# Kernel optimization log

Measured on AMD Instinct MI355X. Metric: run time of the kernel, lower is better.

## Reference

```python
import jax, jax.numpy as jnp
from jax import lax
import numpy as np

S, B, T, N, FJ, H, MF, M = 8, 64, 64, 16, 32, 128, 16, 8
NN = S + M  # total machine-graph nodes
EPS = 1e-5
SLOPE = 0.2


def layernorm(x, g, b):
    mu = x.mean(-1, keepdims=True)
    var = ((x - mu) ** 2).mean(-1, keepdims=True)
    return (x - mu) / jnp.sqrt(var + EPS) * g + b


def gat(adj, x, W, a):
    # dense GAT layer: x [..., N, Fin], adj [..., N, N]
    h = x @ W  # [..., N, O]
    O = W.shape[1]
    f1 = h @ a[:O]  # [..., N]
    f2 = h @ a[O:]
    e = jax.nn.leaky_relu(f1[..., :, None] + f2[..., None, :], SLOPE)
    e = jnp.where(adj > 0, e, jnp.float32(-1e9))
    return jax.nn.softmax(e, axis=-1) @ h


def job_enc(adj, x, Ws, As):
    t = jnp.tanh(gat(adj, x, Ws[0], As[0]))
    t = jnp.tanh(gat(adj, t, Ws[1], As[1]) + t)
    t = jnp.tanh(gat(adj, t, Ws[2], As[2]) + t)
    t = jnp.tanh(t + gat(adj, t, Ws[3], As[3]))
    return t.mean(-2)  # mean over ops dim


def lstm_last(x, Wih, Whh, b):
    # x: [Bx, T, H]; returns final hidden state [Bx, H]
    xs = jnp.einsum('bti,gi->tbg', x, Wih) + b  # [T, Bx, 4H]
    h0 = jnp.zeros((x.shape[0], Whh.shape[1]), x.dtype)

    def step(carry, xt):
        h, c = carry
        g = xt + h @ Whh.T
        i, f, gg, o = jnp.split(g, 4, axis=-1)
        c = jax.nn.sigmoid(f) * c + jax.nn.sigmoid(i) * jnp.tanh(gg)
        h = jax.nn.sigmoid(o) * jnp.tanh(c)
        return (h, c), None

    (h, _), _ = lax.scan(step, (h0, h0), xs)
    return h


def setup_inputs() -> dict:
    key = jax.random.key(0)
    ks = jax.random.split(key, 32)

    def adj(k, shape):
        a = jax.random.bernoulli(k, 0.4, shape).astype(jnp.int32)
        return jnp.maximum(a, jnp.eye(shape[-1], dtype=jnp.int32))

    mfeat = jax.random.normal(ks[4], (B, NN, MF), jnp.float32)
    # stage nodes (first S) have feature[...,0] > 0; machine nodes < 0
    mfeat = mfeat.at[:, :S, 0].set(jnp.abs(mfeat[:, :S, 0]) + 0.1)
    mfeat = mfeat.at[:, S:, 0].set(-jnp.abs(mfeat[:, S:, 0]) - 0.1)

    sc = 0.08
    inp = {
        'j_stages_f': jax.random.normal(ks[0], (S, B, T, N, FJ), jnp.float32),
        'j_stages_a': adj(ks[1], (S, B, T, N, N)),
        'j_machine_f': jax.random.normal(ks[2], (B, M, N, FJ), jnp.float32),
        'j_machine_a': adj(ks[3], (B, M, N, N)),
        'machine_f': mfeat,
        'machine_a': adj(ks[5], (B, NN, NN)),
        'jg1_W': jax.random.normal(ks[6], (FJ, H), jnp.float32) * sc,
        'jgW': jax.random.normal(ks[7], (3, H, H), jnp.float32) * sc,
        'jga': jax.random.normal(ks[8], (4, 2 * H), jnp.float32) * sc,
        'lstm_Wih': jax.random.normal(ks[9], (4 * H, H), jnp.float32) * sc,
        'lstm_Whh': jax.random.normal(ks[10], (4 * H, H), jnp.float32) * sc,
        'lstm_b': jnp.zeros((4 * H,), jnp.float32),
        'mfe_W': jax.random.normal(ks[11], (MF, H), jnp.float32) * sc,
        'mfe_b': jnp.zeros((H,), jnp.float32),
        'n2_g': jnp.ones((H,), jnp.float32),
        'n2_b': jnp.zeros((H,), jnp.float32),
        'me_W': jax.random.normal(ks[12], (2 * H, H), jnp.float32) * sc,
        'me_b': jnp.zeros((H,), jnp.float32),
        'n3_g': jnp.ones((H,), jnp.float32),
        'n3_b': jnp.zeros((H,), jnp.float32),
        'mgW': jax.random.normal(ks[13], (4, H, H), jnp.float32) * sc,
        'mga': jax.random.normal(ks[14], (4, 2 * H), jnp.float32) * sc,
        'mng': jnp.ones((4, H), jnp.float32),
        'mnb': jnp.zeros((4, H), jnp.float32),
    }
    return inp


def reference(j_stages_f, j_stages_a, j_machine_f, j_machine_a, machine_f,
              machine_a, jg1_W, jgW, jga, lstm_Wih, lstm_Whh, lstm_b,
              mfe_W, mfe_b, n2_g, n2_b, me_W, me_b, n3_g, n3_b,
              mgW, mga, mng, mnb):
    Ws = [jg1_W, jgW[0], jgW[1], jgW[2]]
    As = [jga[0], jga[1], jga[2], jga[3]]

    # per-stage job encoding + LSTM over job sequence
    stage_emb = jax.vmap(lambda a, f: job_enc(a, f, Ws, As))(j_stages_a, j_stages_f)  # [S,B,T,H]
    hlast = lstm_last(stage_emb.reshape(S * B, T, H), lstm_Wih, lstm_Whh, lstm_b)
    j_encoded = hlast.reshape(S, B, H).transpose(1, 0, 2)  # [B,S,H]

    # machine-side job graph encoding (shared encoder)
    jm = job_enc(j_machine_a, j_machine_f, Ws, As)  # [B,M,H]

    # machine node embedding
    mfh = jnp.tanh(layernorm(machine_f @ mfe_W + mfe_b, n2_g, n2_b))  # [B,NN,H]

    # static routing: first S nodes -> stage contexts, rest -> machine contexts
    ctx = jnp.concatenate([j_encoded, jm], axis=1)  # [B,NN,H]
    nodes = jnp.concatenate([mfh, ctx], axis=-1)  # [B,NN,2H]
    nodes = jnp.tanh(layernorm(nodes @ me_W + me_b, n3_g, n3_b))

    h = nodes
    prev = None
    for k in range(4):
        h2 = layernorm(gat(machine_a, h, mgW[k], mga[k]), mng[k], mnb[k])
        if k != 0:
            h2 = h2 + prev
        h = jnp.tanh(h2)
        prev = h
    return h.mean(axis=1)  # [B, H]
```

## Files before the change

kernel.cpp:

```cpp
#include <hip/hip_runtime.h>
#include <hip/hip_bf16.h>
#include <math.h>

#define S_ 8
#define B_ 64
#define T_ 64
#define N_ 16
#define FJ_ 32
#define H_ 128
#define MF_ 16
#define M_ 8
#define SB_ 512
#define G1_ 32768
#define G2_ 512

#define CPAD 132
#define PPAD 17

typedef short bf16x8 __attribute__((ext_vector_type(8)));
typedef short bf16x4 __attribute__((ext_vector_type(4)));
typedef float f32x4 __attribute__((ext_vector_type(4)));
typedef unsigned short u16;

__device__ __forceinline__ u16 f2bf(float f) {
  union { float f; unsigned u; } v; v.f = f;
  unsigned r = v.u + 0x7FFFu + ((v.u >> 16) & 1u);
  return (u16)(r >> 16);
}
__device__ __forceinline__ unsigned pk2(float lo, float hi) {
  __hip_bfloat162 h2 = __float22bfloat162_rn(make_float2(lo, hi));
  union { __hip_bfloat162 h; unsigned u; } x; x.h = h2; return x.u;
}
__device__ __forceinline__ bf16x4 mkfrag(unsigned a, unsigned b) {
  union { bf16x4 v; unsigned u[2]; } x; x.u[0] = a; x.u[1] = b; return x.v;
}
__device__ __forceinline__ f32x4 mfma16(bf16x4 a, bf16x4 b, f32x4 c) {
#if __has_builtin(__builtin_amdgcn_mfma_f32_16x16x16bf16_1k)
  return __builtin_amdgcn_mfma_f32_16x16x16bf16_1k(a, b, c, 0, 0, 0);
#else
  asm("v_mfma_f32_16x16x16_bf16 %0, %1, %2, %0" : "+v"(c) : "v"(a), "v"(b));
  return c;
#endif
}
__device__ __forceinline__ float frcp(float x) {
#if __has_builtin(__builtin_amdgcn_rcpf)
  return __builtin_amdgcn_rcpf(x);
#else
  return 1.f / x;
#endif
}
__device__ __forceinline__ float frsq(float x) {
#if __has_builtin(__builtin_amdgcn_rsqf)
  return __builtin_amdgcn_rsqf(x);
#else
  return rsqrtf(x);
#endif
}
__device__ __forceinline__ float ftanh(float x) {
  float e = __expf(2.f * x);
  return fmaf(-2.f, frcp(e + 1.f), 1.f);
}
__device__ __forceinline__ float sigmoidf_(float x) {
  return frcp(1.f + __expf(-x));
}

__device__ __forceinline__ void fma8(float (&acc)[8], float xv, float4 wa, float4 wb) {
  acc[0] = fmaf(xv, wa.x, acc[0]); acc[1] = fmaf(xv, wa.y, acc[1]);
  acc[2] = fmaf(xv, wa.z, acc[2]); acc[3] = fmaf(xv, wa.w, acc[3]);
  acc[4] = fmaf(xv, wb.x, acc[4]); acc[5] = fmaf(xv, wb.y, acc[5]);
  acc[6] = fmaf(xv, wb.z, acc[6]); acc[7] = fmaf(xv, wb.w, acc[7]);
}
__device__ __forceinline__ float grp16_sum(float v) {
#pragma unroll
  for (int m = 1; m < 16; m <<= 1) v += __shfl_xor(v, m);
  return v;
}
__device__ __forceinline__ float grp16_max(float v) {
#pragma unroll
  for (int m = 1; m < 16; m <<= 1) v = fmaxf(v, __shfl_xor(v, m));
  return v;
}
__device__ __forceinline__ void ln_row(float (&v)[8], const float* gw, const float* bw, int j0) {
  float s1 = 0.f, s2 = 0.f;
#pragma unroll
  for (int c = 0; c < 8; ++c) { s1 += v[c]; s2 += v[c] * v[c]; }
  s1 = grp16_sum(s1); s2 = grp16_sum(s2);
  float mu = s1 * (1.f / 128.f);
  float var = s2 * (1.f / 128.f) - mu * mu;
  float rstd = frsq(var + 1e-5f);
#pragma unroll
  for (int c = 0; c < 8; ++c) v[c] = (v[c] - mu) * rstd * gw[j0 + c] + bw[j0 + c];
}

__global__ __launch_bounds__(256) void pack_w_kernel(
    const float* __restrict__ W0, const float* __restrict__ W123,
    const float* __restrict__ jga,
    const float* __restrict__ Wih, const float* __restrict__ Whh,
    u16* __restrict__ wpk0, u16* __restrict__ wpkL,
    u16* __restrict__ wpkIH, u16* __restrict__ wpkHH)
{
  int idx = blockIdx.x * 256 + threadIdx.x;
  if (idx < 4608) {
    int e = idx & 3, l = (idx >> 2) & 63, t = idx >> 8;
    int n = t >> 1, kk = t & 1;
    int q = l >> 4, cc = l & 15;
    int k = 16 * kk + 4 * q + e;
    float v = 0.f;
    if (n < 8) v = W0[k * 128 + 16 * n + cc];
    else if (cc < 2) {
      const float* a = jga + cc * 128;
      float s = 0.f;
      for (int j = 0; j < 128; ++j) s += W0[k * 128 + j] * a[j];
      v = s;
    }
    wpk0[idx] = f2bf(v);
  } else if (idx < 59904) {
    int id = idx - 4608;
    int e = id & 3, l = (id >> 2) & 63;
    int t2 = id >> 8;
    int t = t2 % 72, layer = t2 / 72;
    int n = t >> 3, kk = t & 7;
    int q = l >> 4, cc = l & 15;
    int k = 16 * kk + 4 * q + e;
    const float* W = W123 + (size_t)layer * 16384;
    float v = 0.f;
    if (n < 8) v = W[k * 128 + 16 * n + cc];
    else if (cc < 2) {
      const float* a = jga + (layer + 1) * 256 + cc * 128;
      float s = 0.f;
      for (int j = 0; j < 128; ++j) s += W[k * 128 + j] * a[j];
      v = s;
    }
    wpkL[id] = f2bf(v);
  } else if (idx < 125440) {
    int id = idx - 59904;
    int e = id & 7, l = (id >> 3) & 63, kk = (id >> 9) & 3, n = id >> 11;
    int gate = 16 * n + (l & 15), k = 32 * kk + 8 * (l >> 4) + e;
    wpkIH[id] = f2bf(Wih[gate * 128 + k]);
  } else if (idx < 190976) {
    int id = idx - 125440;
    int e = id & 7, l = (id >> 3) & 63, kk = (id >> 9) & 3, n = id >> 11;
    int gate = 16 * n + (l & 15), k = 32 * kk + 8 * (l >> 4) + e;
    wpkHH[id] = f2bf(Whh[gate * 128 + k]);
  }
}

__global__ __launch_bounds__(512) __attribute__((amdgpu_waves_per_eu(2, 4)))
void gat_mfma_kernel(
    const float* __restrict__ xinA,
    const int* __restrict__ adjA,
    float* __restrict__ outmA, u16* __restrict__ outbfA,
    const float* __restrict__ xinB,
    const int* __restrict__ adjB,
    float* __restrict__ outmB, u16* __restrict__ outbfB,
    const u16* __restrict__ wpk0, const u16* __restrict__ wpkL)
{
  __shared__ __align__(16) u16 wbuf[18432];
  __shared__ __align__(16) float fbuf[8][32];

  const int wv = threadIdx.x >> 6;
  const int l = threadIdx.x & 63;
  const int c = l & 15, q = l >> 4;
  float* fb = fbuf[wv];

  const float* xin; const int* adjin; float* outm; u16* outbf; int g;
  if (blockIdx.x < G1_ / 8) {
    xin = xinA; adjin = adjA; outm = outmA; outbf = outbfA;
    g = blockIdx.x * 8 + wv;
  } else {
    xin = xinB; adjin = adjB; outm = outmB; outbf = outbfB;
    g = (blockIdx.x - G1_ / 8) * 8 + wv;
  }

  auto stage = [&](const u16* src, int nbytes) {
    const float4* s4 = (const float4*)src;
    float4* d4 = (float4*)wbuf;
    int n16 = nbytes >> 4;
    for (int i = threadIdx.x; i < n16; i += 512) d4[i] = s4[i];
  };

  int4 A1 = *(const int4*)(adjin + (size_t)g * 256 + c * 16 + 4 * q);

  f32x4 res[8];
  bf16x4 hfrag[8];

  auto softmax_pv = [&](f32x4 Cf, bool resid) {
    if (c < 2) *(f32x4*)(fb + c * 16 + 4 * q) = Cf;
    float f1v = fb[c];
    float4 f2v = *(const float4*)(fb + 16 + 4 * q);
    float ev[4] = {f1v + f2v.x, f1v + f2v.y, f1v + f2v.z, f1v + f2v.w};
#pragma unroll
    for (int e = 0; e < 4; ++e) ev[e] = (ev[e] >= 0.f) ? ev[e] : 0.2f * ev[e];
    ev[0] = (A1.x > 0) ? ev[0] : -1e9f;
    ev[1] = (A1.y > 0) ? ev[1] : -1e9f;
    ev[2] = (A1.z > 0) ? ev[2] : -1e9f;
    ev[3] = (A1.w > 0) ? ev[3] : -1e9f;
    float mx = fmaxf(fmaxf(ev[0], ev[1]), fmaxf(ev[2], ev[3]));
    mx = fmaxf(mx, __shfl_xor(mx, 16));
    mx = fmaxf(mx, __shfl_xor(mx, 32));
    float sm = 0.f;
#pragma unroll
    for (int e = 0; e < 4; ++e) { ev[e] = __expf(ev[e] - mx); sm += ev[e]; }
    sm += __shfl_xor(sm, 16);
    sm += __shfl_xor(sm, 32);
    float zinv = frcp(sm);
    bf16x4 pfrag = mkfrag(pk2(ev[0] * zinv, ev[1] * zinv), pk2(ev[2] * zinv, ev[3] * zinv));
#pragma unroll
    for (int m = 0; m < 8; ++m) {
      f32x4 o = resid ? res[m] : (f32x4){0.f, 0.f, 0.f, 0.f};
      o = mfma16(hfrag[m], pfrag, o);
      f32x4 t;
      t[0] = ftanh(o[0]); t[1] = ftanh(o[1]); t[2] = ftanh(o[2]); t[3] = ftanh(o[3]);
      res[m] = t;
    }
  };

  stage(wpk0, 9216);
  __syncthreads();
  {
    bf16x4 xf[2];
    const float* xg = xin + (size_t)g * 512 + c * 32 + 4 * q;
    float4 x1 = *(const float4*)xg;
    float4 x2 = *(const float4*)(xg + 16);
    xf[0] = mkfrag(pk2(x1.x, x1.y), pk2(x1.z, x1.w));
    xf[1] = mkfrag(pk2(x2.x, x2.y), pk2(x2.z, x2.w));
#pragma unroll
    for (int n = 0; n < 8; ++n) {
      f32x4 Ch = (f32x4){0.f, 0.f, 0.f, 0.f};
#pragma unroll
      for (int kk = 0; kk < 2; ++kk) {
        bf16x4 wf = *(const bf16x4*)(wbuf + ((n * 2 + kk) * 64 + l) * 4);
        Ch = mfma16(xf[kk], wf, Ch);
      }
      hfrag[n] = mkfrag(pk2(Ch[0], Ch[1]), pk2(Ch[2], Ch[3]));
    }
    f32x4 Cf = (f32x4){0.f, 0.f, 0.f, 0.f};
#pragma unroll
    for (int kk = 0; kk < 2; ++kk) {
      bf16x4 wf = *(const bf16x4*)(wbuf + ((16 + kk) * 64 + l) * 4);
      Cf = mfma16(xf[kk], wf, Cf);
    }
    softmax_pv(Cf, false);
  }
  __syncthreads();

#pragma unroll 1
  for (int layer = 1; layer < 4; ++layer) {
    stage(wpkL + (size_t)(layer - 1) * 18432, 36864);
    __syncthreads();
    bf16x4 xf[8];
#pragma unroll
    for (int kk = 0; kk < 8; ++kk)
      xf[kk] = mkfrag(pk2(res[kk][0], res[kk][1]), pk2(res[kk][2], res[kk][3]));
#pragma unroll
    for (int n = 0; n < 8; ++n) {
      f32x4 Ch = (f32x4){0.f, 0.f, 0.f, 0.f};
#pragma unroll
      for (int kk = 0; kk < 8; ++kk) {
        bf16x4 wf = *(const bf16x4*)(wbuf + ((n * 8 + kk) * 64 + l) * 4);
        Ch = mfma16(xf[kk], wf, Ch);
      }
      hfrag[n] = mkfrag(pk2(Ch[0], Ch[1]), pk2(Ch[2], Ch[3]));
    }
    f32x4 Cf = (f32x4){0.f, 0.f, 0.f, 0.f};
#pragma unroll
    for (int kk = 0; kk < 8; ++kk) {
      bf16x4 wf = *(const bf16x4*)(wbuf + ((64 + kk) * 64 + l) * 4);
      Cf = mfma16(xf[kk], wf, Cf);
    }
    softmax_pv(Cf, true);
    __syncthreads();
  }

  u16* tb = wbuf + wv * 2176;
#pragma unroll
  for (int m = 0; m < 8; ++m) {
    uint2 u;
    u.x = pk2(res[m][0], res[m][1]);
    u.y = pk2(res[m][2], res[m][3]);
    *(uint2*)(tb + c * 136 + 16 * m + 4 * q) = u;
  }
  {
    float s0 = 0.f, s1 = 0.f;
#pragma unroll
    for (int node = 0; node < 16; ++node) {
      unsigned u = *(const unsigned*)(tb + node * 136 + 2 * l);
      union { unsigned u; float f; } lo, hi;
      lo.u = u << 16; hi.u = u & 0xffff0000u;
      s0 += lo.f; s1 += hi.f;
    }
    s0 *= 0.0625f; s1 *= 0.0625f;
    *(float2*)(outm + (size_t)g * 128 + 2 * l) = make_float2(s0, s1);
    *(unsigned*)(outbf + (size_t)g * 128 + 2 * l) = pk2(s0, s1);
  }
}

__global__ __launch_bounds__(512) __attribute__((amdgpu_waves_per_eu(1, 2)))
void lstm_fused_kernel(
    const u16* __restrict__ emb_bf,
    const u16* __restrict__ wpkIH, const u16* __restrict__ wpkHH,
    const float* __restrict__ bvec,
    float* __restrict__ hlast)
{
  __shared__ unsigned hbuf[2][1024];
  const int tid = threadIdx.x;
  const int w = tid >> 6, l = tid & 63;
  const int c = l & 15, q = l >> 4;
  const int seq0 = blockIdx.x * 16;
  const int swz = (c & 7) << 2;

  bf16x8 aih[4][4], ahh[4][4];
#pragma unroll
  for (int m = 0; m < 4; ++m)
#pragma unroll
    for (int kk = 0; kk < 4; ++kk) {
      int n = 8 * m + w;
      aih[m][kk] = *(const bf16x8*)(wpkIH + ((size_t)((n * 4 + kk) * 64 + l)) * 8);
      ahh[m][kk] = *(const bf16x8*)(wpkHH + ((size_t)((n * 4 + kk) * 64 + l)) * 8);
    }
  float bias[4][4];
#pragma unroll
  for (int m = 0; m < 4; ++m)
#pragma unroll
    for (int r = 0; r < 4; ++r) bias[m][r] = bvec[128 * m + 16 * w + 4 * q + r];

  hbuf[0][tid] = 0u;
  hbuf[0][512 + tid] = 0u;
  __syncthreads();

  const u16* xbase = emb_bf + ((size_t)(seq0 + c)) * 64 * 128 + q * 8;

  f32x4 accih[4];
  {
    bf16x8 xf[4];
#pragma unroll
    for (int kk = 0; kk < 4; ++kk) xf[kk] = *(const bf16x8*)(xbase + kk * 32);
#pragma unroll
    for (int m = 0; m < 4; ++m) {
      f32x4 a = (f32x4){0.f, 0.f, 0.f, 0.f};
#pragma unroll
      for (int kk = 0; kk < 4; ++kk)
        a = __builtin_amdgcn_mfma_f32_16x16x32_bf16(aih[m][kk], xf[kk], a, 0, 0, 0);
      accih[m] = a;
    }
  }

  float cst[4] = {0.f, 0.f, 0.f, 0.f};
  float hv[4] = {0.f, 0.f, 0.f, 0.f};
  int pb = 0;
#pragma unroll 1
  for (int t = 0; t < T_; ++t) {
    bf16x8 hf[4];
#pragma unroll
    for (int kk = 0; kk < 4; ++kk) {
      int j0 = (16 * kk + 4 * q) ^ swz;
      hf[kk] = *(const bf16x8*)&hbuf[pb][c * 64 + j0];
    }
    f32x4 acc[4];
#pragma unroll
    for (int m = 0; m < 4; ++m) {
      f32x4 a = accih[m];
#pragma unroll
      for (int kk = 0; kk < 4; ++kk)
        a = __builtin_amdgcn_mfma_f32_16x16x32_bf16(ahh[m][kk], hf[kk], a, 0, 0, 0);
      acc[m] = a;
    }
#pragma unroll
    for (int r = 0; r < 4; ++r) {
      float ig = acc[0][r] + bias[0][r];
      float fg = acc[1][r] + bias[1][r];
      float gg = acc[2][r] + bias[2][r];
      float og = acc[3][r] + bias[3][r];
      cst[r] = sigmoidf_(fg) * cst[r] + sigmoidf_(ig) * ftanh(gg);
      hv[r] = sigmoidf_(og) * ftanh(cst[r]);
    }
    {
      int j0 = (8 * w + 2 * q) ^ swz;
      uint2 u2; u2.x = pk2(hv[0], hv[1]); u2.y = pk2(hv[2], hv[3]);
      *(uint2*)&hbuf[pb ^ 1][c * 64 + j0] = u2;
    }
    __syncthreads();
    pb ^= 1;
    if (t < T_ - 1) {
      bf16x8 xf[4];
      const u16* xr = xbase + (t + 1) * 128;
#pragma unroll
      for (int kk = 0; kk < 4; ++kk) xf[kk] = *(const bf16x8*)(xr + kk * 32);
#pragma unroll
      for (int m = 0; m < 4; ++m) {
        f32x4 a = (f32x4){0.f, 0.f, 0.f, 0.f};
#pragma unroll
        for (int kk = 0; kk < 4; ++kk)
          a = __builtin_amdgcn_mfma_f32_16x16x32_bf16(aih[m][kk], xf[kk], a, 0, 0, 0);
        accih[m] = a;
      }
    }
  }
#pragma unroll
  for (int r = 0; r < 4; ++r)
    hlast[((size_t)(seq0 + c)) * 128 + 16 * w + 4 * q + r] = hv[r];
}

__global__ __launch_bounds__(256) __attribute__((amdgpu_waves_per_eu(2, 4)))
void machine_kernel(
    const float* __restrict__ machine_f, const int* __restrict__ machine_a,
    const float* __restrict__ hlast, const float* __restrict__ jm,
    const float* __restrict__ mfe_W, const float* __restrict__ mfe_b,
    const float* __restrict__ n2_g, const float* __restrict__ n2_b,
    const float* __restrict__ me_W, const float* __restrict__ me_b,
    const float* __restrict__ n3_g, const float* __restrict__ n3_b,
    const float* __restrict__ mgW, const float* __restrict__ mga,
    const float* __restrict__ mng, const float* __restrict__ mnb,
    float* __restrict__ outp)
{
  __shared__ float mf[256];
  __shared__ int adjs[256];
  __shared__ __align__(16) float ctx[16 * CPAD];
  __shared__ __align__(16) float mfh[16 * CPAD];
  __shared__ __align__(16) float cur[16 * CPAD];
  __shared__ __align__(16) float tmp[16 * CPAD];
  __shared__ __align__(16) float prevb[16 * CPAD];
  __shared__ float pm[16 * PPAD];
  __shared__ float f1s[16], f2s[16];

  const int b = blockIdx.x;
  const int tid = threadIdx.x;
  const int i = tid >> 4;
  const int jb = tid & 15;
  const int j0 = jb << 3;

  mf[tid] = machine_f[(size_t)b * 256 + tid];
  adjs[tid] = machine_a[(size_t)b * 256 + tid];
  {
    const float* src = (i < 8) ? (hlast + ((size_t)i * B_ + b) * H_)
                               : (jm + ((size_t)b * M_ + (i - 8)) * H_);
    *(float4*)(ctx + i * CPAD + j0) = ((const float4*)src)[jb * 2];
    *(float4*)(ctx + i * CPAD + j0 + 4) = ((const float4*)src)[jb * 2 + 1];
  }
  __syncthreads();

  {
    float acc[8];
#pragma unroll
    for (int c = 0; c < 8; ++c) acc[c] = 0.f;
#pragma unroll
    for (int k = 0; k < MF_; ++k) {
      float xv = mf[i * 16 + k];
      float4 wa = *(const float4*)(mfe_W + (size_t)k * H_ + j0);
      float4 wb = *(const float4*)(mfe_W + (size_t)k * H_ + j0 + 4);
      fma8(acc, xv, wa, wb);
    }
#pragma unroll
    for (int c = 0; c < 8; ++c) acc[c] += mfe_b[j0 + c];
    ln_row(acc, n2_g, n2_b, j0);
#pragma unroll
    for (int c = 0; c < 8; ++c) mfh[i * CPAD + j0 + c] = ftanh(acc[c]);
  }
  __syncthreads();

  {
    float acc[8];
#pragma unroll
    for (int c = 0; c < 8; ++c) acc[c] = 0.f;
#pragma unroll 4
    for (int k = 0; k < H_; ++k) {
      float xv = mfh[i * CPAD + k];
      float4 wa = *(const float4*)(me_W + (size_t)k * H_ + j0);
      float4 wb = *(const float4*)(me_W + (size_t)k * H_ + j0 + 4);
      fma8(acc, xv, wa, wb);
    }
#pragma unroll 4
    for (int k = 0; k < H_; ++k) {
      float xv = ctx[i * CPAD + k];
      float4 wa = *(const float4*)(me_W + (size_t)(128 + k) * H_ + j0);
      float4 wb = *(const float4*)(me_W + (size_t)(128 + k) * H_ + j0 + 4);
      fma8(acc, xv, wa, wb);
    }
#pragma unroll
    for (int c = 0; c < 8; ++c) acc[c] += me_b[j0 + c];
    ln_row(acc, n3_g, n3_b, j0);
#pragma unroll
    for (int c = 0; c < 8; ++c) cur[i * CPAD + j0 + c] = ftanh(acc[c]);
  }
  __syncthreads();

  for (int l = 0; l < 4; ++l) {
    const float* W = mgW + (size_t)l * H_ * H_;
    const float* a0 = mga + l * 256;
    const float* a1 = a0 + 128;

    float acc[8];
#pragma unroll
    for (int c = 0; c < 8; ++c) acc[c] = 0.f;
#pragma unroll 4
    for (int k = 0; k < H_; ++k) {
      float xv = cur[i * CPAD + k];
      float4 wa = *(const float4*)(W + (size_t)k * H_ + j0);
      float4 wb = *(const float4*)(W + (size_t)k * H_ + j0 + 4);
      fma8(acc, xv, wa, wb);
    }
    *(float4*)(tmp + i * CPAD + j0) = make_float4(acc[0], acc[1], acc[2], acc[3]);
    *(float4*)(tmp + i * CPAD + j0 + 4) = make_float4(acc[4], acc[5], acc[6], acc[7]);

    float p1 = 0.f, p2 = 0.f;
#pragma unroll
    for (int c = 0; c < 8; ++c) {
      p1 = fmaf(acc[c], a0[j0 + c], p1);
      p2 = fmaf(acc[c], a1[j0 + c], p2);
    }
    p1 = grp16_sum(p1); p2 = grp16_sum(p2);
    if (jb == 0) { f1s[i] = p1; f2s[i] = p2; }
    __syncthreads();

    {
      int jc = jb;
      float e = f1s[i] + f2s[jc];
      e = (e >= 0.f) ? e : 0.2f * e;
      if (adjs[i * 16 + jc] <= 0) e = -1e9f;
      float mxv = grp16_max(e);
      float ex = __expf(e - mxv);
      float smv = grp16_sum(ex);
      pm[i * PPAD + jc] = ex * frcp(smv);
    }
    __syncthreads();

    float o[8];
#pragma unroll
    for (int c = 0; c < 8; ++c) o[c] = 0.f;
#pragma unroll
    for (int k = 0; k < 16; ++k) {
      float pv = pm[i * PPAD + k];
      float4 ha = *(const float4*)(tmp + k * CPAD + j0);
      float4 hb = *(const float4*)(tmp + k * CPAD + j0 + 4);
      fma8(o, pv, ha, hb);
    }
    ln_row(o, mng + l * H_, mnb + l * H_, j0);
#pragma unroll
    for (int c = 0; c < 8; ++c) {
      float v = o[c] + ((l > 0) ? prevb[i * CPAD + j0 + c] : 0.f);
      v = ftanh(v);
      cur[i * CPAD + j0 + c] = v;
      prevb[i * CPAD + j0 + c] = v;
    }
    __syncthreads();
  }

  if (tid < 128) {
    float s = 0.f;
#pragma unroll
    for (int r = 0; r < 16; ++r) s += cur[r * CPAD + tid];
    outp[(size_t)b * H_ + tid] = s * (1.f / 16.f);
  }
}

extern "C" void kernel_launch(void* const* d_in, const int* in_sizes, int n_in,
                              void* d_out, int out_size, void* d_ws, size_t ws_size,
                              hipStream_t stream) {
  const float* j_stages_f  = (const float*)d_in[0];
  const int*   j_stages_a  = (const int*)d_in[1];
  const float* j_machine_f = (const float*)d_in[2];
  const int*   j_machine_a = (const int*)d_in[3];
  const float* machine_f   = (const float*)d_in[4];
  const int*   machine_a   = (const int*)d_in[5];
  const float* jg1_W       = (const float*)d_in[6];
  const float* jgW         = (const float*)d_in[7];
  const float* jga         = (const float*)d_in[8];
  const float* lstm_Wih    = (const float*)d_in[9];
  const float* lstm_Whh    = (const float*)d_in[10];
  const float* lstm_b      = (const float*)d_in[11];
  const float* mfe_W       = (const float*)d_in[12];
  const float* mfe_b       = (const float*)d_in[13];
  const float* n2_g        = (const float*)d_in[14];
  const float* n2_b        = (const float*)d_in[15];
  const float* me_W        = (const float*)d_in[16];
  const float* me_b        = (const float*)d_in[17];
  const float* n3_g        = (const float*)d_in[18];
  const float* n3_b        = (const float*)d_in[19];
  const float* mgW         = (const float*)d_in[20];
  const float* mga         = (const float*)d_in[21];
  const float* mng         = (const float*)d_in[22];
  const float* mnb         = (const float*)d_in[23];
  float* out = (float*)d_out;

  char* ws = (char*)d_ws;
  u16*   emb_bf  = (u16*)ws;
  u16*   jmbf    = (u16*)(ws + 8388608);
  float* jm      = (float*)(ws + 8519680);
  float* hlast   = (float*)(ws + 8781824);
  float* outm_s  = (float*)(ws + 9043968);
  u16*   wpk0    = (u16*)(ws + 25821184);
  u16*   wpkL    = (u16*)(ws + 25830400);
  u16*   wpkIH   = (u16*)(ws + 25940992);
  u16*   wpkHH   = (u16*)(ws + 26072064);

  pack_w_kernel<<<746, 256, 0, stream>>>(jg1_W, jgW, jga, lstm_Wih, lstm_Whh,
                                         wpk0, wpkL, wpkIH, wpkHH);
  gat_mfma_kernel<<<G1_ / 8 + G2_ / 8, 512, 0, stream>>>(
      j_stages_f, j_stages_a, outm_s, emb_bf,
      j_machine_f, j_machine_a, jm, jmbf, wpk0, wpkL);
  lstm_fused_kernel<<<SB_ / 16, 512, 0, stream>>>(emb_bf, wpkIH, wpkHH, lstm_b, hlast);
  machine_kernel<<<B_, 256, 0, stream>>>(machine_f, machine_a, hlast, jm,
                                         mfe_W, mfe_b, n2_g, n2_b, me_W, me_b,
                                         n3_g, n3_b, mgW, mga, mng, mnb, out);
}
```

Measured before the change: 368.6 us.

## Halve LSTM sequences per block, prefetch inputs, drop unused fp32 stage output

The LSTM kernel now handles 8 sequences per block instead of 16, launching twice as many blocks to fill more CUs. The MFMA tile columns are duplicated, so half the compute is redundant. Next-step input rows are prefetched one step ahead, and the input-projection MFMAs are issued before the barrier to overlap with synchronisation. The GAT kernel skips the unused fp32 mean-output store for the stage graphs and gets a higher waves-per-EU hint, which may constrain registers.

```diff
diff --git a/kernel.cpp b/kernel.cpp
--- a/kernel.cpp
+++ b/kernel.cpp
@@ -145,13 +145,11 @@
   }
 }
 
-__global__ __launch_bounds__(512) __attribute__((amdgpu_waves_per_eu(2, 4)))
+__global__ __launch_bounds__(512) __attribute__((amdgpu_waves_per_eu(4, 8)))
 void gat_mfma_kernel(
-    const float* __restrict__ xinA,
-    const int* __restrict__ adjA,
+    const float* __restrict__ xinA, const int* __restrict__ adjA,
     float* __restrict__ outmA, u16* __restrict__ outbfA,
-    const float* __restrict__ xinB,
-    const int* __restrict__ adjB,
+    const float* __restrict__ xinB, const int* __restrict__ adjB,
     float* __restrict__ outmB, u16* __restrict__ outbfB,
     const u16* __restrict__ wpk0, const u16* __restrict__ wpkL)
 {
@@ -290,7 +288,7 @@
       s0 += lo.f; s1 += hi.f;
     }
     s0 *= 0.0625f; s1 *= 0.0625f;
-    *(float2*)(outm + (size_t)g * 128 + 2 * l) = make_float2(s0, s1);
+    if (outm) *(float2*)(outm + (size_t)g * 128 + 2 * l) = make_float2(s0, s1);
     *(unsigned*)(outbf + (size_t)g * 128 + 2 * l) = pk2(s0, s1);
   }
 }
@@ -306,7 +304,8 @@
   const int tid = threadIdx.x;
   const int w = tid >> 6, l = tid & 63;
   const int c = l & 15, q = l >> 4;
-  const int seq0 = blockIdx.x * 16;
+  const int ce = c & 7;
+  const int seq0 = blockIdx.x * 8;
   const int swz = (c & 7) << 2;
 
   bf16x8 aih[4][4], ahh[4][4];
@@ -328,8 +327,9 @@
   hbuf[0][512 + tid] = 0u;
   __syncthreads();
 
-  const u16* xbase = emb_bf + ((size_t)(seq0 + c)) * 64 * 128 + q * 8;
-
+  const u16* xbase = emb_bf + ((size_t)(seq0 + ce)) * 64 * 128 + q * 8;
+
+  bf16x8 xnxt[4];
   f32x4 accih[4];
   {
     bf16x8 xf[4];
@@ -343,6 +343,8 @@
         a = __builtin_amdgcn_mfma_f32_16x16x32_bf16(aih[m][kk], xf[kk], a, 0, 0, 0);
       accih[m] = a;
     }
+#pragma unroll
+    for (int kk = 0; kk < 4; ++kk) xnxt[kk] = *(const bf16x8*)(xbase + 128 + kk * 32);
   }
 
   float cst[4] = {0.f, 0.f, 0.f, 0.f};
@@ -379,26 +381,29 @@
       uint2 u2; u2.x = pk2(hv[0], hv[1]); u2.y = pk2(hv[2], hv[3]);
       *(uint2*)&hbuf[pb ^ 1][c * 64 + j0] = u2;
     }
+    if (t < T_ - 1) {
+#pragma unroll
+      for (int m = 0; m < 4; ++m) {
+        f32x4 a = (f32x4){0.f, 0.f, 0.f, 0.f};
+#pragma unroll
+        for (int kk = 0; kk < 4; ++kk)
+          a = __builtin_amdgcn_mfma_f32_16x16x32_bf16(aih[m][kk], xnxt[kk], a, 0, 0, 0);
+        accih[m] = a;
+      }
+      if (t < T_ - 2) {
+        const u16* xr = xbase + (size_t)(t + 2) * 128;
+#pragma unroll
+        for (int kk = 0; kk < 4; ++kk) xnxt[kk] = *(const bf16x8*)(xr + kk * 32);
+      }
+    }
     __syncthreads();
     pb ^= 1;
-    if (t < T_ - 1) {
-      bf16x8 xf[4];
-      const u16* xr = xbase + (t + 1) * 128;
-#pragma unroll
-      for (int kk = 0; kk < 4; ++kk) xf[kk] = *(const bf16x8*)(xr + kk * 32);
-#pragma unroll
-      for (int m = 0; m < 4; ++m) {
-        f32x4 a = (f32x4){0.f, 0.f, 0.f, 0.f};
-#pragma unroll
-        for (int kk = 0; kk < 4; ++kk)
-          a = __builtin_amdgcn_mfma_f32_16x16x32_bf16(aih[m][kk], xf[kk], a, 0, 0, 0);
-        accih[m] = a;
-      }
-    }
-  }
-#pragma unroll
-  for (int r = 0; r < 4; ++r)
-    hlast[((size_t)(seq0 + c)) * 128 + 16 * w + 4 * q + r] = hv[r];
+  }
+  if (c < 8) {
+#pragma unroll
+    for (int r = 0; r < 4; ++r)
+      hlast[((size_t)(seq0 + ce)) * 128 + 16 * w + 4 * q + r] = hv[r];
+  }
 }
 
 __global__ __launch_bounds__(256) __attribute__((amdgpu_waves_per_eu(2, 4)))
@@ -484,9 +489,9 @@
   }
   __syncthreads();
 
-  for (int l = 0; l < 4; ++l) {
-    const float* W = mgW + (size_t)l * H_ * H_;
-    const float* a0 = mga + l * 256;
+  for (int ll = 0; ll < 4; ++ll) {
+    const float* W = mgW + (size_t)ll * H_ * H_;
+    const float* a0 = mga + ll * 256;
     const float* a1 = a0 + 128;
 
     float acc[8];
@@ -534,10 +539,10 @@
       float4 hb = *(const float4*)(tmp + k * CPAD + j0 + 4);
       fma8(o, pv, ha, hb);
     }
-    ln_row(o, mng + l * H_, mnb + l * H_, j0);
+    ln_row(o, mng + ll * H_, mnb + ll * H_, j0);
 #pragma unroll
     for (int c = 0; c < 8; ++c) {
-      float v = o[c] + ((l > 0) ? prevb[i * CPAD + j0 + c] : 0.f);
+      float v = o[c] + ((ll > 0) ? prevb[i * CPAD + j0 + c] : 0.f);
       v = ftanh(v);
       cur[i * CPAD + j0 + c] = v;
       prevb[i * CPAD + j0 + c] = v;
@@ -587,18 +592,17 @@
   u16*   jmbf    = (u16*)(ws + 8388608);
   float* jm      = (float*)(ws + 8519680);
   float* hlast   = (float*)(ws + 8781824);
-  float* outm_s  = (float*)(ws + 9043968);
-  u16*   wpk0    = (u16*)(ws + 25821184);
-  u16*   wpkL    = (u16*)(ws + 25830400);
-  u16*   wpkIH   = (u16*)(ws + 25940992);
-  u16*   wpkHH   = (u16*)(ws + 26072064);
+  u16*   wpk0    = (u16*)(ws + 9043968);
+  u16*   wpkL    = (u16*)(ws + 9053184);
+  u16*   wpkIH   = (u16*)(ws + 9163776);
+  u16*   wpkHH   = (u16*)(ws + 9294848);
 
   pack_w_kernel<<<746, 256, 0, stream>>>(jg1_W, jgW, jga, lstm_Wih, lstm_Whh,
                                          wpk0, wpkL, wpkIH, wpkHH);
   gat_mfma_kernel<<<G1_ / 8 + G2_ / 8, 512, 0, stream>>>(
-      j_stages_f, j_stages_a, outm_s, emb_bf,
+      j_stages_f, j_stages_a, (float*)nullptr, emb_bf,
       j_machine_f, j_machine_a, jm, jmbf, wpk0, wpkL);
-  lstm_fused_kernel<<<SB_ / 16, 512, 0, stream>>>(emb_bf, wpkIH, wpkHH, lstm_b, hlast);
+  lstm_fused_kernel<<<SB_ / 8, 512, 0, stream>>>(emb_bf, wpkIH, wpkHH, lstm_b, hlast);
   machine_kernel<<<B_, 256, 0, stream>>>(machine_f, machine_a, hlast, jm,
                                          mfe_W, mfe_b, n2_g, n2_b, me_W, me_b,
                                          n3_g, n3_b, mgW, mga, mng, mnb, out);
```

Result: faster. 325.8 us (-11.6%).
